# Performance work log

Hardware: AMD Instinct MI355X
Metric: run time of the kernel (lower is better)

The kernel has to match this reference:

```python
import jax, jax.numpy as jnp
import numpy as np

BETA = 0.25
ENT_MULT = 0.1
COMMIT_MULT = 0.1


def setup_inputs() -> dict:
    key = jax.random.key(0)
    z = jax.random.normal(key, (64, 13, 128, 128), dtype=jnp.float32)
    return {"z": z}


def reference(z):
    B, C, H, W = z.shape
    # (B,C,H,W) -> (B,H,W,C) -> (N,C)
    zf = jnp.transpose(z, (0, 2, 3, 1)).reshape(-1, C)
    # binary sign quantization (>0 -> +1, else -1) with straight-through estimator
    q = jnp.where(zf > 0, 1.0, -1.0).astype(zf.dtype)
    z_q = zf + jax.lax.stop_gradient(q - zf)
    # Categorical over logits [-(z-1)^2, -(z+1)^2] per latent dim; shape (N,C,2)
    logits = jnp.stack([-(zf - 1.0) ** 2, -(zf + 1.0) ** 2], axis=-1)
    logp = jax.nn.log_softmax(logits, axis=-1)
    p = jnp.exp(logp)
    entropy = jnp.mean(-(p * logp).sum(-1))          # per-sample entropy, averaged
    mean_prob = p.mean(0)                              # (C,2), rows already sum to 1
    mean_entropy = jnp.mean(-(mean_prob * jnp.log(mean_prob)).sum(-1))
    # commitment loss (both directions, beta-weighted)
    commit_loss = jnp.mean((jax.lax.stop_gradient(z_q) - zf) ** 2) \
        + BETA * jnp.mean((z_q - jax.lax.stop_gradient(zf)) ** 2)
    # back to (B,C,H,W)
    z_q4 = jnp.transpose(z_q.reshape(B, H, W, C), (0, 3, 1, 2))
    # bit-pack indices: MSB = channel 0
    powers = (2 ** jnp.arange(C - 1, -1, -1)).astype(jnp.float32)  # (C,)
    indices = (powers.reshape(1, -1, 1, 1) * (z_q4 > 0).astype(jnp.float32)) \
        .sum(axis=1, keepdims=True).astype(jnp.int32)              # (B,1,H,W)
    return (z_q4,
            commit_loss * COMMIT_MULT,
            (entropy - mean_entropy) * ENT_MULT,
            indices)
```

## Files before the change

kernel.cpp:

```cpp
#include <hip/hip_runtime.h>
#include <math.h>

constexpr int B = 64;
constexpr int C = 13;
constexpr int HW = 128 * 128;
constexpr long long NTOT = (long long)B * C * HW;
constexpr long long NSAMP = (long long)B * HW;

constexpr long long COMMIT_OFF = NTOT;
constexpr long long ENT_OFF = NTOT + 1;
constexpr long long IDX_OFF = NTOT + 2;

constexpr int THREADS = 256;
constexpr int VEC = 2;
constexpr int CHUNK = THREADS * VEC;
constexpr int BLOCKS_PER_B = HW / CHUNK;
constexpr int NACC = 15;

__global__ __launch_bounds__(THREADS, 8) void lfq_main(const float* __restrict__ z,
                                                       float* __restrict__ out,
                                                       double* __restrict__ acc) {
    constexpr float kLog2e4 = 5.7707801635558535f;
    constexpr float kLn2 = 0.6931471805599453f;

    const int bid = blockIdx.x;
    const int b = bid / BLOCKS_PER_B;
    const int j = bid % BLOCKS_PER_B;
    const int hw0 = j * CHUNK + (int)threadIdx.x * VEC;

    float cm_s = 0.0f;
    float ent_s = 0.0f;
    float p0_s[C];
#pragma unroll
    for (int c = 0; c < C; ++c) p0_s[c] = 0.0f;
    int idx[VEC] = {0, 0};

    const float* zb = z + (size_t)b * C * HW + hw0;
    float* zq = out + (size_t)b * C * HW + hw0;

#pragma unroll
    for (int c = 0; c < C; ++c) {
        const float2 v = *reinterpret_cast<const float2*>(zb + (size_t)c * HW);
        float zz[VEC] = {v.x, v.y};
        float qq[VEC];
#pragma unroll
        for (int k = 0; k < VEC; ++k) {
            const float zv = zz[k];
            const bool pos = (zv > 0.0f);
            qq[k] = pos ? 1.0f : -1.0f;
            const float az = fabsf(zv);
            const float dm = az - 1.0f;
            cm_s = fmaf(dm, dm, cm_s);
            const float e = __builtin_amdgcn_exp2f(-kLog2e4 * az);
            const float ope = 1.0f + e;
            const float sp = __builtin_amdgcn_logf(ope) * kLn2;
            const float ps = e * __builtin_amdgcn_rcpf(ope);
            ent_s += fmaf(4.0f * az, ps, sp);
            p0_s[c] += pos ? (1.0f - ps) : ps;
            if (pos) idx[k] |= (1 << (C - 1 - c));
        }
        float2 qv;
        qv.x = qq[0]; qv.y = qq[1];
        *reinterpret_cast<float2*>(zq + (size_t)c * HW) = qv;
    }

    float2 fi;
    fi.x = (float)idx[0]; fi.y = (float)idx[1];
    *reinterpret_cast<float2*>(out + IDX_OFF + (size_t)b * HW + hw0) = fi;

    float vals[NACC];
    vals[0] = cm_s;
    vals[1] = ent_s;
#pragma unroll
    for (int c = 0; c < C; ++c) vals[2 + c] = p0_s[c];
#pragma unroll
    for (int off = 32; off > 0; off >>= 1) {
#pragma unroll
        for (int k = 0; k < NACC; ++k) vals[k] += __shfl_down(vals[k], off);
    }
    __shared__ float red[THREADS / 64][NACC];
    const int wave = threadIdx.x >> 6;
    const int lane = threadIdx.x & 63;
    if (lane == 0) {
#pragma unroll
        for (int k = 0; k < NACC; ++k) red[wave][k] = vals[k];
    }
    __syncthreads();
    if (threadIdx.x < NACC) {
        double s = 0.0;
#pragma unroll
        for (int w = 0; w < THREADS / 64; ++w) s += (double)red[w][threadIdx.x];
        atomicAdd(&acc[threadIdx.x], s);
    }
}

__global__ void lfq_final(const double* __restrict__ acc, float* __restrict__ out) {
    if (threadIdx.x == 0 && blockIdx.x == 0) {
        const double commit = acc[0] / (double)NTOT;
        const double ent = acc[1] / (double)NTOT;
        double me = 0.0;
        for (int c = 0; c < C; ++c) {
            const double mp0 = acc[2 + c] / (double)NSAMP;
            const double mp1 = 1.0 - mp0;
            me += -(mp0 * log(mp0) + mp1 * log(mp1));
        }
        me /= (double)C;
        out[COMMIT_OFF] = (float)(0.1 * 1.25 * commit);
        out[ENT_OFF] = (float)(0.1 * (ent - me));
    }
}

extern "C" void kernel_launch(void* const* d_in, const int* in_sizes, int n_in,
                              void* d_out, int out_size, void* d_ws, size_t ws_size,
                              hipStream_t stream) {
    const float* z = (const float*)d_in[0];
    float* out = (float*)d_out;
    double* acc = (double*)d_ws;

    hipMemsetAsync(d_ws, 0, NACC * sizeof(double), stream);
    lfq_main<<<B * BLOCKS_PER_B, THREADS, 0, stream>>>(z, out, acc);
    lfq_final<<<1, 64, 0, stream>>>(acc, out);
}
```

Baseline: 128.1 us.

## Widen to float4 and replace double atomics with per-block partials plus final reduction

Each thread now processes four pixels with float4 loads and stores instead of two, halving the block count to 1024. The double-precision atomicAdd accumulation and the memset are replaced by per-block float partials written to workspace. The final kernel launches 1024 threads to reduce them in one block. This removes atomic contention and a memset launch, at the cost of more registers per thread (launch bounds relaxed) and float rather than double summation within each block.

```diff
diff --git a/kernel.cpp b/kernel.cpp
--- a/kernel.cpp
+++ b/kernel.cpp
@@ -12,14 +12,16 @@
 constexpr long long IDX_OFF = NTOT + 2;
 
 constexpr int THREADS = 256;
-constexpr int VEC = 2;
+constexpr int VEC = 4;
 constexpr int CHUNK = THREADS * VEC;
 constexpr int BLOCKS_PER_B = HW / CHUNK;
+constexpr int NBLK = B * BLOCKS_PER_B;
 constexpr int NACC = 15;
+constexpr int SLOT = 16;
 
-__global__ __launch_bounds__(THREADS, 8) void lfq_main(const float* __restrict__ z,
+__global__ __launch_bounds__(THREADS, 4) void lfq_main(const float* __restrict__ z,
                                                        float* __restrict__ out,
-                                                       double* __restrict__ acc) {
+                                                       float* __restrict__ part) {
     constexpr float kLog2e4 = 5.7707801635558535f;
     constexpr float kLn2 = 0.6931471805599453f;
 
@@ -33,15 +35,15 @@
     float p0_s[C];
 #pragma unroll
     for (int c = 0; c < C; ++c) p0_s[c] = 0.0f;
-    int idx[VEC] = {0, 0};
+    int idx[VEC] = {0, 0, 0, 0};
 
     const float* zb = z + (size_t)b * C * HW + hw0;
     float* zq = out + (size_t)b * C * HW + hw0;
 
 #pragma unroll
     for (int c = 0; c < C; ++c) {
-        const float2 v = *reinterpret_cast<const float2*>(zb + (size_t)c * HW);
-        float zz[VEC] = {v.x, v.y};
+        const float4 v = *reinterpret_cast<const float4*>(zb + (size_t)c * HW);
+        float zz[VEC] = {v.x, v.y, v.z, v.w};
         float qq[VEC];
 #pragma unroll
         for (int k = 0; k < VEC; ++k) {
@@ -59,14 +61,14 @@
             p0_s[c] += pos ? (1.0f - ps) : ps;
             if (pos) idx[k] |= (1 << (C - 1 - c));
         }
-        float2 qv;
-        qv.x = qq[0]; qv.y = qq[1];
-        *reinterpret_cast<float2*>(zq + (size_t)c * HW) = qv;
+        float4 qv;
+        qv.x = qq[0]; qv.y = qq[1]; qv.z = qq[2]; qv.w = qq[3];
+        *reinterpret_cast<float4*>(zq + (size_t)c * HW) = qv;
     }
 
-    float2 fi;
-    fi.x = (float)idx[0]; fi.y = (float)idx[1];
-    *reinterpret_cast<float2*>(out + IDX_OFF + (size_t)b * HW + hw0) = fi;
+    float4 fi;
+    fi.x = (float)idx[0]; fi.y = (float)idx[1]; fi.z = (float)idx[2]; fi.w = (float)idx[3];
+    *reinterpret_cast<float4*>(out + IDX_OFF + (size_t)b * HW + hw0) = fi;
 
     float vals[NACC];
     vals[0] = cm_s;
@@ -87,15 +89,42 @@
     }
     __syncthreads();
     if (threadIdx.x < NACC) {
-        double s = 0.0;
+        float s = 0.0f;
 #pragma unroll
-        for (int w = 0; w < THREADS / 64; ++w) s += (double)red[w][threadIdx.x];
-        atomicAdd(&acc[threadIdx.x], s);
+        for (int w = 0; w < THREADS / 64; ++w) s += red[w][threadIdx.x];
+        part[(size_t)bid * SLOT + threadIdx.x] = s;
     }
 }
 
-__global__ void lfq_final(const double* __restrict__ acc, float* __restrict__ out) {
-    if (threadIdx.x == 0 && blockIdx.x == 0) {
+__global__ __launch_bounds__(NBLK) void lfq_final(const float* __restrict__ part,
+                                                  float* __restrict__ out) {
+    const int t = threadIdx.x;
+    float vals[NACC];
+    const float* p = part + (size_t)t * SLOT;
+#pragma unroll
+    for (int k = 0; k < NACC; ++k) vals[k] = p[k];
+#pragma unroll
+    for (int off = 32; off > 0; off >>= 1) {
+#pragma unroll
+        for (int k = 0; k < NACC; ++k) vals[k] += __shfl_down(vals[k], off);
+    }
+    __shared__ float red[NBLK / 64][NACC];
+    const int wave = t >> 6;
+    const int lane = t & 63;
+    if (lane == 0) {
+#pragma unroll
+        for (int k = 0; k < NACC; ++k) red[wave][k] = vals[k];
+    }
+    __syncthreads();
+    if (t == 0) {
+        double acc[NACC];
+#pragma unroll
+        for (int k = 0; k < NACC; ++k) {
+            double s = 0.0;
+#pragma unroll
+            for (int w = 0; w < NBLK / 64; ++w) s += (double)red[w][k];
+            acc[k] = s;
+        }
         const double commit = acc[0] / (double)NTOT;
         const double ent = acc[1] / (double)NTOT;
         double me = 0.0;
@@ -115,9 +144,8 @@
                               hipStream_t stream) {
     const float* z = (const float*)d_in[0];
     float* out = (float*)d_out;
-    double* acc = (double*)d_ws;
+    float* part = (float*)d_ws;
 
-    hipMemsetAsync(d_ws, 0, NACC * sizeof(double), stream);
-    lfq_main<<<B * BLOCKS_PER_B, THREADS, 0, stream>>>(z, out, acc);
-    lfq_final<<<1, 64, 0, stream>>>(acc, out);
+    lfq_main<<<NBLK, THREADS, 0, stream>>>(z, out, part);
+    lfq_final<<<1, NBLK, 0, stream>>>(part, out);
 }
```

New measurement: 115.3 us. 1.11x faster.
